# Kernel tuning notes

Hardware: AMD Instinct MI355X
Metric: run time of the kernel (lower is better)

The kernel has to match this reference:

```python
import jax, jax.numpy as jnp
import numpy as np

N = 100000   # nodes
R = 6        # relations (edge types)
E = 400000   # edges per relation
F_IN = 128   # metapath2vec embedding dim
HID = 128    # hidden_dim (conv1 out == conv2 out in RGCN)
OUT = 2      # out_size


def setup_inputs() -> dict:
    key = jax.random.key(0)
    ks = jax.random.split(key, 9)
    x = jax.random.normal(ks[0], (N, F_IN), dtype=jnp.float32)
    edge_src = jax.random.randint(ks[1], (R, E), 0, N, dtype=jnp.int32)
    edge_dst = jax.random.randint(ks[2], (R, E), 0, N, dtype=jnp.int32)
    W1 = jax.random.normal(ks[3], (R, F_IN, HID), dtype=jnp.float32) * 0.05
    b1 = jnp.zeros((R, HID), dtype=jnp.float32)
    W2 = jax.random.normal(ks[4], (R, HID, HID), dtype=jnp.float32) * 0.05
    b2 = jnp.zeros((R, HID), dtype=jnp.float32)
    Wc = jax.random.normal(ks[5], (HID, OUT), dtype=jnp.float32) * 0.05
    bc = jnp.zeros((OUT,), dtype=jnp.float32)
    return {"x": x, "edge_src": edge_src, "edge_dst": edge_dst,
            "W1": W1, "b1": b1, "W2": W2, "b2": b2, "Wc": Wc, "bc": bc}


def _graph_conv(x, src, dst, W, b):
    """DGL GraphConv, norm='both': D_dst^{-1/2} A D_src^{-1/2} X W + b."""
    ones = jnp.ones(src.shape, x.dtype)
    deg_out = jax.ops.segment_sum(ones, src, num_segments=N)  # [N]
    deg_in = jax.ops.segment_sum(ones, dst, num_segments=N)   # [N]
    norm_src = jnp.where(deg_out > 0, jax.lax.rsqrt(jnp.maximum(deg_out, 1.0)), 0.0)
    norm_dst = jnp.where(deg_in > 0, jax.lax.rsqrt(jnp.maximum(deg_in, 1.0)), 0.0)
    msg = (x * norm_src[:, None])[src]                         # [E, F] gather
    agg = jax.ops.segment_sum(msg, dst, num_segments=N)       # [N, F] scatter-sum
    return (agg * norm_dst[:, None]) @ W + b                  # [N, H]


def _hetero_layer(x, edge_src, edge_dst, W, b):
    # HeteroGraphConv(aggregate='sum'): run each relation's GraphConv, sum results.
    conv = jax.vmap(_graph_conv, in_axes=(None, 0, 0, 0, 0))
    return conv(x, edge_src, edge_dst, W, b).sum(axis=0)      # [N, H]


def reference(x, edge_src, edge_dst, W1, b1, W2, b2, Wc, bc):
    h = jax.nn.relu(_hetero_layer(x, edge_src, edge_dst, W1, b1))
    h = _hetero_layer(h, edge_src, edge_dst, W2, b2)
    g = h.mean(axis=0)          # mean-pool node embeddings -> graph embedding
    return g @ Wc + bc          # classifier logits, shape [OUT]
```

## Files before the change

kernel.cpp:

```cpp
#include <hip/hip_runtime.h>

#define N_NODES 100000
#define NREL 6
#define NEDGE 400000
#define FDIM 128
#define HID 128

constexpr int RN = NREL * N_NODES;
constexpr int NBIN = 391;
constexpr int BINCAP = 1280;
constexpr int CSRCAP = 2304;
constexpr int CHUNK = 8192;
constexpr int NCHUNK = (NEDGE + CHUNK - 1) / CHUNK;

constexpr int NB_XC = (N_NODES * 32) / 256;
constexpr int NB_WC = (NREL * FDIM * HID) / 256;
constexpr int PREP_BLOCKS = NB_XC + NB_WC + NREL + 1;

typedef __attribute__((ext_vector_type(8))) short short8;
typedef __attribute__((ext_vector_type(4))) float f32x4;

__device__ __forceinline__ unsigned short f2bf(float f) {
  union { float f; unsigned int u; } v; v.f = f;
  unsigned int u = v.u;
  unsigned int r = (u + 0x7FFFu + ((u >> 16) & 1u)) >> 16;
  return (unsigned short)r;
}
__device__ __forceinline__ float bflo(unsigned int w) {
  union { unsigned int u; float f; } v; v.u = w << 16; return v.f;
}
__device__ __forceinline__ float bfhi(unsigned int w) {
  union { unsigned int u; float f; } v; v.u = w & 0xffff0000u; return v.f;
}

__global__ void k_zero(unsigned int* __restrict__ p, int nwords) {
  int id = blockIdx.x * blockDim.x + threadIdx.x;
  if (id < nwords) p[id] = 0u;
}

__global__ __launch_bounds__(256) void k_phase1(
    const int* __restrict__ src, const int* __restrict__ dst,
    int* __restrict__ gCurIn, int* __restrict__ gCurOut,
    unsigned int* __restrict__ stIn, unsigned int* __restrict__ stOut) {
  __shared__ int hIn[NBIN], hOut[NBIN], bIn[NBIN], bOut[NBIN];
  const int r = blockIdx.x / NCHUNK;
  const int c = blockIdx.x % NCHUNK;
  const int t = threadIdx.x;
  for (int i = t; i < NBIN; i += 256) { hIn[i] = 0; hOut[i] = 0; }
  __syncthreads();
  const int base = c * CHUNK;
  const int lim = min(CHUNK, NEDGE - base);
  const int* __restrict__ sR = src + r * NEDGE + base;
  const int* __restrict__ dR = dst + r * NEDGE + base;
  for (int i = t; i < lim; i += 256) {
    atomicAdd(&hIn[dR[i] >> 8], 1);
    atomicAdd(&hOut[sR[i] >> 8], 1);
  }
  __syncthreads();
  for (int i = t; i < NBIN; i += 256) {
    bIn[i]  = atomicAdd(&gCurIn[r * NBIN + i], hIn[i]);
    bOut[i] = atomicAdd(&gCurOut[r * NBIN + i], hOut[i]);
    hIn[i] = 0; hOut[i] = 0;
  }
  __syncthreads();
  for (int i = t; i < lim; i += 256) {
    const int s = sR[i], d = dR[i];
    const int bi = d >> 8, bo = s >> 8;
    const int pi = bIn[bi] + atomicAdd(&hIn[bi], 1);
    const int po = bOut[bo] + atomicAdd(&hOut[bo], 1);
    if (pi < BINCAP)
      stIn[(size_t)(r * NBIN + bi) * BINCAP + pi] = ((unsigned)(d & 255) << 17) | (unsigned)s;
    if (po < BINCAP)
      stOut[(size_t)(r * NBIN + bo) * BINCAP + po] = ((unsigned)(s & 255) << 17) | (unsigned)d;
  }
}

__global__ __launch_bounds__(256) void k_p2a(const unsigned int* __restrict__ stOut,
                                             const int* __restrict__ gCurOut,
                                             float* __restrict__ ns) {
  __shared__ int cnt[256];
  const int rb = blockIdx.x;
  const int r = rb / NBIN, b = rb % NBIN;
  const int t = threadIdx.x;
  cnt[t] = 0;
  __syncthreads();
  const int m = min(gCurOut[rb], BINCAP);
  const unsigned int* __restrict__ st = stOut + (size_t)rb * BINCAP;
  for (int i = t; i < m; i += 256) atomicAdd(&cnt[st[i] >> 17], 1);
  __syncthreads();
  const int n = b * 256 + t;
  if (n < N_NODES) ns[r * N_NODES + n] = cnt[t] > 0 ? rsqrtf((float)cnt[t]) : 0.f;
}

__global__ __launch_bounds__(256) void k_p2in(const unsigned int* __restrict__ stIn,
                                              const int* __restrict__ gCurIn,
                                              const float* __restrict__ ns,
                                              int4* __restrict__ meta,
                                              float* __restrict__ ndA,
                                              int2* __restrict__ csr) {
  __shared__ int cnt[256], offs[256];
  __shared__ int wsum[4];
  const int rb = blockIdx.x;
  const int r = rb / NBIN, b = rb % NBIN;
  const int t = threadIdx.x;
  cnt[t] = 0;
  __syncthreads();
  const int m = min(gCurIn[rb], BINCAP);
  const unsigned int* __restrict__ st = stIn + (size_t)rb * BINCAP;
  for (int i = t; i < m; i += 256) atomicAdd(&cnt[st[i] >> 17], 1);
  __syncthreads();
  const int lane = t & 63, wid = t >> 6;
  const int pc = (cnt[t] + 3) & ~3;
  int sum = pc;
#pragma unroll
  for (int o = 1; o < 64; o <<= 1) {
    int y = __shfl_up(sum, o);
    if (lane >= o) sum += y;
  }
  if (lane == 63) wsum[wid] = sum;
  __syncthreads();
  int wadd = 0;
  for (int w = 0; w < wid; ++w) wadd += wsum[w];
  offs[t] = sum - pc + wadd;
  __syncthreads();
  const int n = b * 256 + t;
  const int binBase = rb * CSRCAP;
  if (n < N_NODES) {
    const int d = cnt[t];
    const float nd = d > 0 ? rsqrtf((float)d) : 0.f;
    meta[r * N_NODES + n] = make_int4(d, binBase + offs[t], __float_as_int(nd), 0);
    ndA[r * N_NODES + n] = nd;
    int2* __restrict__ c = csr + binBase + offs[t];
    for (int e = d; e < ((d + 3) & ~3); ++e) c[e] = make_int2(0, 0);
  }
  __syncthreads();
  cnt[t] = 0;
  __syncthreads();
  const float* __restrict__ nsr = ns + r * N_NODES;
  for (int i = t; i < m; i += 256) {
    const unsigned int v = st[i];
    const int local = v >> 17;
    const int s = v & 0x1FFFF;
    const int pos = offs[local] + atomicAdd(&cnt[local], 1);
    csr[binBase + pos] = make_int2(s, __float_as_int(nsr[s]));
  }
}

__global__ __launch_bounds__(256) void k_p2b(const unsigned int* __restrict__ stOut,
                                             const int* __restrict__ gCurOut,
                                             const float* __restrict__ ns,
                                             const float* __restrict__ ndA,
                                             float* __restrict__ wmv) {
  __shared__ float fc[256];
  const int rb = blockIdx.x;
  const int r = rb / NBIN, b = rb % NBIN;
  const int t = threadIdx.x;
  fc[t] = 0.f;
  __syncthreads();
  const int m = min(gCurOut[rb], BINCAP);
  const unsigned int* __restrict__ st = stOut + (size_t)rb * BINCAP;
  const float* __restrict__ ndr = ndA + r * N_NODES;
  for (int i = t; i < m; i += 256) {
    const unsigned int v = st[i];
    atomicAdd(&fc[v >> 17], ndr[v & 0x1FFFF]);
  }
  __syncthreads();
  const int n = b * 256 + t;
  if (n < N_NODES) {
    const int rn = r * N_NODES + n;
    wmv[rn] = fc[t] * ns[rn];
  }
}

__global__ __launch_bounds__(256) void k_prep(
    const float* __restrict__ x, unsigned short* __restrict__ xb,
    const float* __restrict__ W1, const float* __restrict__ b1,
    const float* __restrict__ b2,
    unsigned short* __restrict__ W1T, float* __restrict__ bias1,
    float* __restrict__ bias2,
    const float* __restrict__ W2, const float* __restrict__ Wc,
    float* __restrict__ u) {
  const int b = blockIdx.x;
  const int t = threadIdx.x;
  if (b < NB_XC) {
    const int id = b * 256 + t;
    const float4 v = ((const float4*)x)[id];
    ushort4 o;
    o.x = f2bf(v.x); o.y = f2bf(v.y); o.z = f2bf(v.z); o.w = f2bf(v.w);
    ((ushort4*)xb)[id] = o;
  } else if (b < NB_XC + NB_WC) {
    const int id = (b - NB_XC) * 256 + t;
    const int r = id >> 14;
    const int rem = id & 16383;
    const int j = rem >> 7;
    const int k = rem & 127;
    W1T[id] = f2bf(W1[r * 16384 + k * 128 + j]);
  } else if (b < NB_XC + NB_WC + NREL) {
    const int r = b - (NB_XC + NB_WC);
    const int k = t >> 1;
    const int c = t & 1;
    const float* __restrict__ row = W2 + r * (HID * HID) + k * HID;
    float s = 0.f;
#pragma unroll 8
    for (int j = 0; j < HID; ++j) s = fmaf(row[j], Wc[j * 2 + c], s);
    u[(r * HID + k) * 2 + c] = s;
  } else {
    if (t < HID) {
      float s1 = 0.f, s2 = 0.f;
      for (int r = 0; r < NREL; ++r) {
        s1 += b1[r * HID + t];
        s2 += b2[r * HID + t];
      }
      bias1[t] = s1;
      bias2[t] = s2;
    }
  }
}

__global__ __launch_bounds__(256, 6) void k_layer1(
    const unsigned short* __restrict__ xb,
    const int2* __restrict__ csr_ew,
    const int4* __restrict__ meta,
    const unsigned short* __restrict__ W1T,
    const float* __restrict__ bias1,
    unsigned short* __restrict__ h)
{
  __shared__ unsigned short zA[4][16][136];
  const int tid = threadIdx.x;
  const int wave = tid >> 6;
  const int lane = tid & 63;
  const int sub = lane >> 4;
  const int flane = lane & 15;
  const int wnb = blockIdx.x * 64 + wave * 16;

  f32x4 acc[8];
#pragma unroll
  for (int t = 0; t < 8; ++t) acc[t] = (f32x4){0.f, 0.f, 0.f, 0.f};

  const int pn = wnb + flane;
  const bool pok = pn < N_NODES;
  const int pnc = pok ? pn : (N_NODES - 1);
  int4 mt = meta[pnc];
  if (!pok) { mt.x = 0; mt.z = 0; }

  for (int r = 0; r < NREL; ++r) {
#pragma unroll
    for (int pass = 0; pass < 4; ++pass) {
      const int row = pass * 4 + sub;
      const int d = __shfl(mt.x, row);
      const int o = __shfl(mt.y, row);
      const float nd = __int_as_float(__shfl(mt.z, row));
      const uint4* __restrict__ lst = (const uint4*)(csr_ew + o);
      const unsigned fo = (unsigned)(flane << 3);
      float b[8];
#pragma unroll
      for (int k = 0; k < 8; ++k) b[k] = 0.f;
      const int nb = (d + 3) >> 2;
      for (int bi = 0; bi < nb; ++bi) {
        const uint4 qa = lst[2 * bi];
        const uint4 qb = lst[2 * bi + 1];
        const float w0 = __uint_as_float(qa.y);
        const float w1 = __uint_as_float(qa.w);
        const float w2 = __uint_as_float(qb.y);
        const float w3 = __uint_as_float(qb.w);
        const uint4 v0 = *(const uint4*)(xb + ((size_t)qa.x << 7) + fo);
        const uint4 v1 = *(const uint4*)(xb + ((size_t)qa.z << 7) + fo);
        const uint4 v2 = *(const uint4*)(xb + ((size_t)qb.x << 7) + fo);
        const uint4 v3 = *(const uint4*)(xb + ((size_t)qb.z << 7) + fo);
#define ACC8(V, W) \
        b[0] = fmaf(bflo(V.x), W, b[0]); b[1] = fmaf(bfhi(V.x), W, b[1]); \
        b[2] = fmaf(bflo(V.y), W, b[2]); b[3] = fmaf(bfhi(V.y), W, b[3]); \
        b[4] = fmaf(bflo(V.z), W, b[4]); b[5] = fmaf(bfhi(V.z), W, b[5]); \
        b[6] = fmaf(bflo(V.w), W, b[6]); b[7] = fmaf(bfhi(V.w), W, b[7]);
        ACC8(v0, w0) ACC8(v1, w1) ACC8(v2, w2) ACC8(v3, w3)
#undef ACC8
      }
      uint4 pk;
      pk.x = (unsigned)f2bf(b[0] * nd) | ((unsigned)f2bf(b[1] * nd) << 16);
      pk.y = (unsigned)f2bf(b[2] * nd) | ((unsigned)f2bf(b[3] * nd) << 16);
      pk.z = (unsigned)f2bf(b[4] * nd) | ((unsigned)f2bf(b[5] * nd) << 16);
      pk.w = (unsigned)f2bf(b[6] * nd) | ((unsigned)f2bf(b[7] * nd) << 16);
      *(uint4*)(&zA[wave][row][flane * 8]) = pk;
    }
    int4 mtn = mt;
    if (r + 1 < NREL) {
      mtn = meta[(r + 1) * N_NODES + pnc];
      if (!pok) { mtn.x = 0; mtn.z = 0; }
    }
    const int m = lane & 15;
    const int qq = lane >> 4;
    const unsigned short* __restrict__ wr = W1T + r * (FDIM * HID);
#pragma unroll
    for (int kk = 0; kk < 4; ++kk) {
      const short8 af = *(const short8*)(&zA[wave][m][kk * 32 + qq * 8]);
#pragma unroll
      for (int t = 0; t < 8; ++t) {
        const short8 bfr = *(const short8*)(wr + (t * 16 + m) * 128 + kk * 32 + qq * 8);
        acc[t] = __builtin_amdgcn_mfma_f32_16x16x32_bf16(af, bfr, acc[t], 0, 0, 0);
      }
    }
    mt = mtn;
  }
  const int col = lane & 15;
  const int rq = (lane >> 4) * 4;
#pragma unroll
  for (int t = 0; t < 8; ++t) {
#pragma unroll
    for (int rr = 0; rr < 4; ++rr) {
      const int node = wnb + rq + rr;
      if (node < N_NODES) {
        const int f = t * 16 + col;
        float v = acc[t][rr] + bias1[f];
        v = fmaxf(v, 0.f);
        h[(size_t)node * FDIM + f] = f2bf(v);
      }
    }
  }
}

__global__ __launch_bounds__(256) void k_mv(const unsigned short* __restrict__ h,
                                            const float* __restrict__ wmv,
                                            float* __restrict__ mv) {
  __shared__ float sh[16][136];
  const int sub = threadIdx.x >> 4;
  const int flane = threadIdx.x & 15;
  const unsigned fo = (unsigned)(flane << 3);
  float acc[NREL][8];
#pragma unroll
  for (int r = 0; r < NREL; ++r)
#pragma unroll
    for (int k = 0; k < 8; ++k) acc[r][k] = 0.f;
  const int nbase = blockIdx.x * 256 + sub * 16;
  for (int i = 0; i < 16; ++i) {
    const int n = nbase + i;
    if (n >= N_NODES) break;
    const uint4 hv = *(const uint4*)(h + ((size_t)n << 7) + fo);
    float hf[8];
    hf[0] = bflo(hv.x); hf[1] = bfhi(hv.x); hf[2] = bflo(hv.y); hf[3] = bfhi(hv.y);
    hf[4] = bflo(hv.z); hf[5] = bfhi(hv.z); hf[6] = bflo(hv.w); hf[7] = bfhi(hv.w);
#pragma unroll
    for (int r = 0; r < NREL; ++r) {
      const float w = wmv[r * N_NODES + n];
#pragma unroll
      for (int k = 0; k < 8; ++k) acc[r][k] = fmaf(w, hf[k], acc[r][k]);
    }
  }
  const float inv = 1.0f / (float)N_NODES;
  const int t = threadIdx.x;
#pragma unroll
  for (int r = 0; r < NREL; ++r) {
    __syncthreads();
#pragma unroll
    for (int k = 0; k < 8; ++k) sh[sub][flane * 8 + k] = acc[r][k];
    __syncthreads();
    if (t < 128) {
      float s = 0.f;
#pragma unroll
      for (int j = 0; j < 16; ++j) s += sh[j][t];
      atomicAdd(&mv[r * HID + t], s * inv);
    }
  }
}

__global__ __launch_bounds__(256) void k_final(const float* __restrict__ mv,
                                               const float* __restrict__ u,
                                               const float* __restrict__ bias2,
                                               const float* __restrict__ Wc,
                                               const float* __restrict__ bc,
                                               float* __restrict__ out) {
  __shared__ float r0[256], r1[256];
  const int t = threadIdx.x;
  float s0 = 0.f, s1 = 0.f;
  for (int rk = t; rk < NREL * HID; rk += 256) {
    const float m = mv[rk];
    s0 = fmaf(m, u[rk * 2], s0);
    s1 = fmaf(m, u[rk * 2 + 1], s1);
  }
  r0[t] = s0; r1[t] = s1;
  __syncthreads();
  for (int off = 128; off > 0; off >>= 1) {
    if (t < off) { r0[t] += r0[t + off]; r1[t] += r1[t + off]; }
    __syncthreads();
  }
  if (t == 0) {
    float t0 = bc[0], t1 = bc[1];
    for (int j = 0; j < HID; ++j) {
      const float b = bias2[j];
      t0 = fmaf(b, Wc[j * 2], t0);
      t1 = fmaf(b, Wc[j * 2 + 1], t1);
    }
    out[0] = r0[0] + t0;
    out[1] = r1[0] + t1;
  }
}

extern "C" void kernel_launch(void* const* d_in, const int* in_sizes, int n_in,
                              void* d_out, int out_size, void* d_ws, size_t ws_size,
                              hipStream_t stream) {
  (void)in_sizes; (void)n_in; (void)out_size; (void)ws_size;
  const float* x   = (const float*)d_in[0];
  const int* esrc  = (const int*)d_in[1];
  const int* edst  = (const int*)d_in[2];
  const float* W1  = (const float*)d_in[3];
  const float* b1  = (const float*)d_in[4];
  const float* W2  = (const float*)d_in[5];
  const float* b2  = (const float*)d_in[6];
  const float* Wc  = (const float*)d_in[7];
  const float* bc  = (const float*)d_in[8];
  float* out = (float*)d_out;

  char* p = (char*)d_ws;
  size_t off = 0;
  auto take = [&](size_t bytes) -> void* {
    void* q = p + off;
    off += (bytes + 255) & ~(size_t)255;
    return q;
  };
  int*   gCurIn  = (int*)take((size_t)NREL * NBIN * 4);
  int*   gCurOut = (int*)take((size_t)NREL * NBIN * 4);
  float* mv      = (float*)take((size_t)NREL * HID * 4);
  const size_t zero_bytes = off;
  float* ns   = (float*)take((size_t)RN * 4);
  float* ndA  = (float*)take((size_t)RN * 4);
  float* wmv  = (float*)take((size_t)RN * 4);
  int4*  meta = (int4*)take((size_t)RN * 16);
  unsigned int* stIn  = (unsigned int*)take((size_t)NREL * NBIN * BINCAP * 4);
  unsigned int* stOut = (unsigned int*)take((size_t)NREL * NBIN * BINCAP * 4);
  int2* csr = (int2*)take((size_t)NREL * NBIN * CSRCAP * 8);
  unsigned short* W1T = (unsigned short*)take((size_t)NREL * FDIM * HID * 2);
  float* bias1 = (float*)take(HID * 4);
  float* bias2 = (float*)take(HID * 4);
  float* u     = (float*)take((size_t)NREL * HID * 2 * 4);
  unsigned short* h  = (unsigned short*)take((size_t)N_NODES * FDIM * 2);
  unsigned short* xb = (unsigned short*)take((size_t)N_NODES * FDIM * 2);

  const int zero_words = (int)(zero_bytes / 4);
  k_zero<<<(zero_words + 255) / 256, 256, 0, stream>>>((unsigned int*)d_ws, zero_words);
  k_phase1<<<NREL * NCHUNK, 256, 0, stream>>>(esrc, edst, gCurIn, gCurOut, stIn, stOut);
  k_p2a<<<NREL * NBIN, 256, 0, stream>>>(stOut, gCurOut, ns);
  k_p2in<<<NREL * NBIN, 256, 0, stream>>>(stIn, gCurIn, ns, meta, ndA, csr);
  k_p2b<<<NREL * NBIN, 256, 0, stream>>>(stOut, gCurOut, ns, ndA, wmv);
  k_prep<<<PREP_BLOCKS, 256, 0, stream>>>(x, xb, W1, b1, b2, W1T, bias1, bias2, W2, Wc, u);
  k_layer1<<<(N_NODES + 63) / 64, 256, 0, stream>>>(xb, csr, meta, W1T, bias1, h);
  k_mv<<<(N_NODES + 255) / 256, 256, 0, stream>>>(h, wmv, mv);
  k_final<<<1, 256, 0, stream>>>(mv, u, bias2, Wc, bc, out);
}
```

Before: 590.9 us.

## Fuse graph-build kernels and shrink layer1 blocks to single waves

Merges the edge-binning phase into the prep kernel, so both run as one launch with heterogeneous blocks. The separate out-degree, in-CSR and weight passes become two kernels: one computes both degree counts plus CSR offsets, the other fills the CSR and the wmv weights. Layer1 now launches one 64-thread wave per 16 nodes and drops the bounds checks, which relies on N being divisible by 16. This cuts the number of launches and repeated bin scans and gives finer block scheduling for layer1.

```diff
diff --git a/kernel.cpp b/kernel.cpp
--- a/kernel.cpp
+++ b/kernel.cpp
@@ -13,9 +13,10 @@
 constexpr int CHUNK = 8192;
 constexpr int NCHUNK = (NEDGE + CHUNK - 1) / CHUNK;
 
+constexpr int PH1_BLOCKS = NREL * NCHUNK;
 constexpr int NB_XC = (N_NODES * 32) / 256;
 constexpr int NB_WC = (NREL * FDIM * HID) / 256;
-constexpr int PREP_BLOCKS = NB_XC + NB_WC + NREL + 1;
+constexpr int BUILD_BLOCKS = PH1_BLOCKS + NB_XC + NB_WC + NREL + 1;
 
 typedef __attribute__((ext_vector_type(8))) short short8;
 typedef __attribute__((ext_vector_type(4))) float f32x4;
@@ -38,141 +39,10 @@
   if (id < nwords) p[id] = 0u;
 }
 
-__global__ __launch_bounds__(256) void k_phase1(
+__global__ __launch_bounds__(256) void k_build(
     const int* __restrict__ src, const int* __restrict__ dst,
     int* __restrict__ gCurIn, int* __restrict__ gCurOut,
-    unsigned int* __restrict__ stIn, unsigned int* __restrict__ stOut) {
-  __shared__ int hIn[NBIN], hOut[NBIN], bIn[NBIN], bOut[NBIN];
-  const int r = blockIdx.x / NCHUNK;
-  const int c = blockIdx.x % NCHUNK;
-  const int t = threadIdx.x;
-  for (int i = t; i < NBIN; i += 256) { hIn[i] = 0; hOut[i] = 0; }
-  __syncthreads();
-  const int base = c * CHUNK;
-  const int lim = min(CHUNK, NEDGE - base);
-  const int* __restrict__ sR = src + r * NEDGE + base;
-  const int* __restrict__ dR = dst + r * NEDGE + base;
-  for (int i = t; i < lim; i += 256) {
-    atomicAdd(&hIn[dR[i] >> 8], 1);
-    atomicAdd(&hOut[sR[i] >> 8], 1);
-  }
-  __syncthreads();
-  for (int i = t; i < NBIN; i += 256) {
-    bIn[i]  = atomicAdd(&gCurIn[r * NBIN + i], hIn[i]);
-    bOut[i] = atomicAdd(&gCurOut[r * NBIN + i], hOut[i]);
-    hIn[i] = 0; hOut[i] = 0;
-  }
-  __syncthreads();
-  for (int i = t; i < lim; i += 256) {
-    const int s = sR[i], d = dR[i];
-    const int bi = d >> 8, bo = s >> 8;
-    const int pi = bIn[bi] + atomicAdd(&hIn[bi], 1);
-    const int po = bOut[bo] + atomicAdd(&hOut[bo], 1);
-    if (pi < BINCAP)
-      stIn[(size_t)(r * NBIN + bi) * BINCAP + pi] = ((unsigned)(d & 255) << 17) | (unsigned)s;
-    if (po < BINCAP)
-      stOut[(size_t)(r * NBIN + bo) * BINCAP + po] = ((unsigned)(s & 255) << 17) | (unsigned)d;
-  }
-}
-
-__global__ __launch_bounds__(256) void k_p2a(const unsigned int* __restrict__ stOut,
-                                             const int* __restrict__ gCurOut,
-                                             float* __restrict__ ns) {
-  __shared__ int cnt[256];
-  const int rb = blockIdx.x;
-  const int r = rb / NBIN, b = rb % NBIN;
-  const int t = threadIdx.x;
-  cnt[t] = 0;
-  __syncthreads();
-  const int m = min(gCurOut[rb], BINCAP);
-  const unsigned int* __restrict__ st = stOut + (size_t)rb * BINCAP;
-  for (int i = t; i < m; i += 256) atomicAdd(&cnt[st[i] >> 17], 1);
-  __syncthreads();
-  const int n = b * 256 + t;
-  if (n < N_NODES) ns[r * N_NODES + n] = cnt[t] > 0 ? rsqrtf((float)cnt[t]) : 0.f;
-}
-
-__global__ __launch_bounds__(256) void k_p2in(const unsigned int* __restrict__ stIn,
-                                              const int* __restrict__ gCurIn,
-                                              const float* __restrict__ ns,
-                                              int4* __restrict__ meta,
-                                              float* __restrict__ ndA,
-                                              int2* __restrict__ csr) {
-  __shared__ int cnt[256], offs[256];
-  __shared__ int wsum[4];
-  const int rb = blockIdx.x;
-  const int r = rb / NBIN, b = rb % NBIN;
-  const int t = threadIdx.x;
-  cnt[t] = 0;
-  __syncthreads();
-  const int m = min(gCurIn[rb], BINCAP);
-  const unsigned int* __restrict__ st = stIn + (size_t)rb * BINCAP;
-  for (int i = t; i < m; i += 256) atomicAdd(&cnt[st[i] >> 17], 1);
-  __syncthreads();
-  const int lane = t & 63, wid = t >> 6;
-  const int pc = (cnt[t] + 3) & ~3;
-  int sum = pc;
-#pragma unroll
-  for (int o = 1; o < 64; o <<= 1) {
-    int y = __shfl_up(sum, o);
-    if (lane >= o) sum += y;
-  }
-  if (lane == 63) wsum[wid] = sum;
-  __syncthreads();
-  int wadd = 0;
-  for (int w = 0; w < wid; ++w) wadd += wsum[w];
-  offs[t] = sum - pc + wadd;
-  __syncthreads();
-  const int n = b * 256 + t;
-  const int binBase = rb * CSRCAP;
-  if (n < N_NODES) {
-    const int d = cnt[t];
-    const float nd = d > 0 ? rsqrtf((float)d) : 0.f;
-    meta[r * N_NODES + n] = make_int4(d, binBase + offs[t], __float_as_int(nd), 0);
-    ndA[r * N_NODES + n] = nd;
-    int2* __restrict__ c = csr + binBase + offs[t];
-    for (int e = d; e < ((d + 3) & ~3); ++e) c[e] = make_int2(0, 0);
-  }
-  __syncthreads();
-  cnt[t] = 0;
-  __syncthreads();
-  const float* __restrict__ nsr = ns + r * N_NODES;
-  for (int i = t; i < m; i += 256) {
-    const unsigned int v = st[i];
-    const int local = v >> 17;
-    const int s = v & 0x1FFFF;
-    const int pos = offs[local] + atomicAdd(&cnt[local], 1);
-    csr[binBase + pos] = make_int2(s, __float_as_int(nsr[s]));
-  }
-}
-
-__global__ __launch_bounds__(256) void k_p2b(const unsigned int* __restrict__ stOut,
-                                             const int* __restrict__ gCurOut,
-                                             const float* __restrict__ ns,
-                                             const float* __restrict__ ndA,
-                                             float* __restrict__ wmv) {
-  __shared__ float fc[256];
-  const int rb = blockIdx.x;
-  const int r = rb / NBIN, b = rb % NBIN;
-  const int t = threadIdx.x;
-  fc[t] = 0.f;
-  __syncthreads();
-  const int m = min(gCurOut[rb], BINCAP);
-  const unsigned int* __restrict__ st = stOut + (size_t)rb * BINCAP;
-  const float* __restrict__ ndr = ndA + r * N_NODES;
-  for (int i = t; i < m; i += 256) {
-    const unsigned int v = st[i];
-    atomicAdd(&fc[v >> 17], ndr[v & 0x1FFFF]);
-  }
-  __syncthreads();
-  const int n = b * 256 + t;
-  if (n < N_NODES) {
-    const int rn = r * N_NODES + n;
-    wmv[rn] = fc[t] * ns[rn];
-  }
-}
-
-__global__ __launch_bounds__(256) void k_prep(
+    unsigned int* __restrict__ stIn, unsigned int* __restrict__ stOut,
     const float* __restrict__ x, unsigned short* __restrict__ xb,
     const float* __restrict__ W1, const float* __restrict__ b1,
     const float* __restrict__ b2,
@@ -180,23 +50,54 @@
     float* __restrict__ bias2,
     const float* __restrict__ W2, const float* __restrict__ Wc,
     float* __restrict__ u) {
-  const int b = blockIdx.x;
+  __shared__ int hIn[NBIN], hOut[NBIN], bIn[NBIN], bOut[NBIN];
+  const int blk = blockIdx.x;
   const int t = threadIdx.x;
-  if (b < NB_XC) {
-    const int id = b * 256 + t;
+  if (blk < PH1_BLOCKS) {
+    const int r = blk / NCHUNK;
+    const int c = blk % NCHUNK;
+    for (int i = t; i < NBIN; i += 256) { hIn[i] = 0; hOut[i] = 0; }
+    __syncthreads();
+    const int base = c * CHUNK;
+    const int lim = min(CHUNK, NEDGE - base);
+    const int* __restrict__ sR = src + r * NEDGE + base;
+    const int* __restrict__ dR = dst + r * NEDGE + base;
+    for (int i = t; i < lim; i += 256) {
+      atomicAdd(&hIn[dR[i] >> 8], 1);
+      atomicAdd(&hOut[sR[i] >> 8], 1);
+    }
+    __syncthreads();
+    for (int i = t; i < NBIN; i += 256) {
+      bIn[i]  = atomicAdd(&gCurIn[r * NBIN + i], hIn[i]);
+      bOut[i] = atomicAdd(&gCurOut[r * NBIN + i], hOut[i]);
+      hIn[i] = 0; hOut[i] = 0;
+    }
+    __syncthreads();
+    for (int i = t; i < lim; i += 256) {
+      const int s = sR[i], d = dR[i];
+      const int bi = d >> 8, bo = s >> 8;
+      const int pi = bIn[bi] + atomicAdd(&hIn[bi], 1);
+      const int po = bOut[bo] + atomicAdd(&hOut[bo], 1);
+      if (pi < BINCAP)
+        stIn[(size_t)(r * NBIN + bi) * BINCAP + pi] = ((unsigned)(d & 255) << 17) | (unsigned)s;
+      if (po < BINCAP)
+        stOut[(size_t)(r * NBIN + bo) * BINCAP + po] = ((unsigned)(s & 255) << 17) | (unsigned)d;
+    }
+  } else if (blk < PH1_BLOCKS + NB_XC) {
+    const int id = (blk - PH1_BLOCKS) * 256 + t;
     const float4 v = ((const float4*)x)[id];
     ushort4 o;
     o.x = f2bf(v.x); o.y = f2bf(v.y); o.z = f2bf(v.z); o.w = f2bf(v.w);
     ((ushort4*)xb)[id] = o;
-  } else if (b < NB_XC + NB_WC) {
-    const int id = (b - NB_XC) * 256 + t;
+  } else if (blk < PH1_BLOCKS + NB_XC + NB_WC) {
+    const int id = (blk - PH1_BLOCKS - NB_XC) * 256 + t;
     const int r = id >> 14;
     const int rem = id & 16383;
     const int j = rem >> 7;
     const int k = rem & 127;
     W1T[id] = f2bf(W1[r * 16384 + k * 128 + j]);
-  } else if (b < NB_XC + NB_WC + NREL) {
-    const int r = b - (NB_XC + NB_WC);
+  } else if (blk < PH1_BLOCKS + NB_XC + NB_WC + NREL) {
+    const int r = blk - (PH1_BLOCKS + NB_XC + NB_WC);
     const int k = t >> 1;
     const int c = t & 1;
     const float* __restrict__ row = W2 + r * (HID * HID) + k * HID;
@@ -217,7 +118,101 @@
   }
 }
 
-__global__ __launch_bounds__(256, 6) void k_layer1(
+__global__ __launch_bounds__(256) void k_p2cnt(const unsigned int* __restrict__ stIn,
+                                               const unsigned int* __restrict__ stOut,
+                                               const int* __restrict__ gCurIn,
+                                               const int* __restrict__ gCurOut,
+                                               float* __restrict__ ns,
+                                               float* __restrict__ ndA,
+                                               int4* __restrict__ meta,
+                                               int2* __restrict__ csr) {
+  __shared__ int cntIn[256], cntOut[256];
+  __shared__ int wsum[4];
+  const int rb = blockIdx.x;
+  const int r = rb / NBIN, b = rb % NBIN;
+  const int t = threadIdx.x;
+  cntIn[t] = 0; cntOut[t] = 0;
+  __syncthreads();
+  const int mi = min(gCurIn[rb], BINCAP);
+  const int mo = min(gCurOut[rb], BINCAP);
+  const unsigned int* __restrict__ sti = stIn + (size_t)rb * BINCAP;
+  const unsigned int* __restrict__ sto = stOut + (size_t)rb * BINCAP;
+  for (int i = t; i < mi; i += 256) atomicAdd(&cntIn[sti[i] >> 17], 1);
+  for (int i = t; i < mo; i += 256) atomicAdd(&cntOut[sto[i] >> 17], 1);
+  __syncthreads();
+  const int lane = t & 63, wid = t >> 6;
+  const int pc = (cntIn[t] + 3) & ~3;
+  int sum = pc;
+#pragma unroll
+  for (int o = 1; o < 64; o <<= 1) {
+    int y = __shfl_up(sum, o);
+    if (lane >= o) sum += y;
+  }
+  if (lane == 63) wsum[wid] = sum;
+  __syncthreads();
+  int wadd = 0;
+  for (int w = 0; w < wid; ++w) wadd += wsum[w];
+  const int off = sum - pc + wadd;
+  const int n = b * 256 + t;
+  const int binBase = rb * CSRCAP;
+  if (n < N_NODES) {
+    const int rn = r * N_NODES + n;
+    const int d = cntIn[t];
+    const int dO = cntOut[t];
+    const float nd = d > 0 ? rsqrtf((float)d) : 0.f;
+    ns[rn] = dO > 0 ? rsqrtf((float)dO) : 0.f;
+    ndA[rn] = nd;
+    meta[rn] = make_int4(d, binBase + off, __float_as_int(nd), 0);
+    int2* __restrict__ c = csr + binBase + off;
+    for (int e = d; e < ((d + 3) & ~3); ++e) c[e] = make_int2(0, 0);
+  }
+}
+
+__global__ __launch_bounds__(256) void k_p2fill(const unsigned int* __restrict__ stIn,
+                                                const unsigned int* __restrict__ stOut,
+                                                const int* __restrict__ gCurIn,
+                                                const int* __restrict__ gCurOut,
+                                                const int4* __restrict__ meta,
+                                                const float* __restrict__ ns,
+                                                const float* __restrict__ ndA,
+                                                int2* __restrict__ csr,
+                                                float* __restrict__ wmv) {
+  __shared__ int offs[256], cnt[256];
+  __shared__ float fc[256];
+  const int rb = blockIdx.x;
+  const int r = rb / NBIN, b = rb % NBIN;
+  const int t = threadIdx.x;
+  const int n = b * 256 + t;
+  const int rnT = r * N_NODES + (n < N_NODES ? n : N_NODES - 1);
+  offs[t] = meta[rnT].y;
+  cnt[t] = 0;
+  fc[t] = 0.f;
+  __syncthreads();
+  const int mi = min(gCurIn[rb], BINCAP);
+  const int mo = min(gCurOut[rb], BINCAP);
+  const unsigned int* __restrict__ sti = stIn + (size_t)rb * BINCAP;
+  const unsigned int* __restrict__ sto = stOut + (size_t)rb * BINCAP;
+  const float* __restrict__ nsr = ns + r * N_NODES;
+  const float* __restrict__ ndr = ndA + r * N_NODES;
+  for (int i = t; i < mi; i += 256) {
+    const unsigned int v = sti[i];
+    const int local = v >> 17;
+    const int s = v & 0x1FFFF;
+    const int pos = offs[local] + atomicAdd(&cnt[local], 1);
+    csr[pos] = make_int2(s, __float_as_int(nsr[s]));
+  }
+  for (int i = t; i < mo; i += 256) {
+    const unsigned int v = sto[i];
+    atomicAdd(&fc[v >> 17], ndr[v & 0x1FFFF]);
+  }
+  __syncthreads();
+  if (n < N_NODES) {
+    const int rn = r * N_NODES + n;
+    wmv[rn] = fc[t] * ns[rn];
+  }
+}
+
+__global__ __launch_bounds__(64, 8) void k_layer1(
     const unsigned short* __restrict__ xb,
     const int2* __restrict__ csr_ew,
     const int4* __restrict__ meta,
@@ -225,23 +220,18 @@
     const float* __restrict__ bias1,
     unsigned short* __restrict__ h)
 {
-  __shared__ unsigned short zA[4][16][136];
-  const int tid = threadIdx.x;
-  const int wave = tid >> 6;
-  const int lane = tid & 63;
+  __shared__ unsigned short zA[16][136];
+  const int lane = threadIdx.x;
   const int sub = lane >> 4;
   const int flane = lane & 15;
-  const int wnb = blockIdx.x * 64 + wave * 16;
+  const int wnb = blockIdx.x * 16;
 
   f32x4 acc[8];
 #pragma unroll
   for (int t = 0; t < 8; ++t) acc[t] = (f32x4){0.f, 0.f, 0.f, 0.f};
 
   const int pn = wnb + flane;
-  const bool pok = pn < N_NODES;
-  const int pnc = pok ? pn : (N_NODES - 1);
-  int4 mt = meta[pnc];
-  if (!pok) { mt.x = 0; mt.z = 0; }
+  int4 mt = meta[pn];
 
   for (int r = 0; r < NREL; ++r) {
 #pragma unroll
@@ -280,19 +270,16 @@
       pk.y = (unsigned)f2bf(b[2] * nd) | ((unsigned)f2bf(b[3] * nd) << 16);
       pk.z = (unsigned)f2bf(b[4] * nd) | ((unsigned)f2bf(b[5] * nd) << 16);
       pk.w = (unsigned)f2bf(b[6] * nd) | ((unsigned)f2bf(b[7] * nd) << 16);
-      *(uint4*)(&zA[wave][row][flane * 8]) = pk;
+      *(uint4*)(&zA[row][flane * 8]) = pk;
     }
     int4 mtn = mt;
-    if (r + 1 < NREL) {
-      mtn = meta[(r + 1) * N_NODES + pnc];
-      if (!pok) { mtn.x = 0; mtn.z = 0; }
-    }
+    if (r + 1 < NREL) mtn = meta[(r + 1) * N_NODES + pn];
     const int m = lane & 15;
     const int qq = lane >> 4;
     const unsigned short* __restrict__ wr = W1T + r * (FDIM * HID);
 #pragma unroll
     for (int kk = 0; kk < 4; ++kk) {
-      const short8 af = *(const short8*)(&zA[wave][m][kk * 32 + qq * 8]);
+      const short8 af = *(const short8*)(&zA[m][kk * 32 + qq * 8]);
 #pragma unroll
       for (int t = 0; t < 8; ++t) {
         const short8 bfr = *(const short8*)(wr + (t * 16 + m) * 128 + kk * 32 + qq * 8);
@@ -308,12 +295,10 @@
 #pragma unroll
     for (int rr = 0; rr < 4; ++rr) {
       const int node = wnb + rq + rr;
-      if (node < N_NODES) {
-        const int f = t * 16 + col;
-        float v = acc[t][rr] + bias1[f];
-        v = fmaxf(v, 0.f);
-        h[(size_t)node * FDIM + f] = f2bf(v);
-      }
+      const int f = t * 16 + col;
+      float v = acc[t][rr] + bias1[f];
+      v = fmaxf(v, 0.f);
+      h[(size_t)node * FDIM + f] = f2bf(v);
     }
   }
 }
@@ -436,12 +421,14 @@
 
   const int zero_words = (int)(zero_bytes / 4);
   k_zero<<<(zero_words + 255) / 256, 256, 0, stream>>>((unsigned int*)d_ws, zero_words);
-  k_phase1<<<NREL * NCHUNK, 256, 0, stream>>>(esrc, edst, gCurIn, gCurOut, stIn, stOut);
-  k_p2a<<<NREL * NBIN, 256, 0, stream>>>(stOut, gCurOut, ns);
-  k_p2in<<<NREL * NBIN, 256, 0, stream>>>(stIn, gCurIn, ns, meta, ndA, csr);
-  k_p2b<<<NREL * NBIN, 256, 0, stream>>>(stOut, gCurOut, ns, ndA, wmv);
-  k_prep<<<PREP_BLOCKS, 256, 0, stream>>>(x, xb, W1, b1, b2, W1T, bias1, bias2, W2, Wc, u);
-  k_layer1<<<(N_NODES + 63) / 64, 256, 0, stream>>>(xb, csr, meta, W1T, bias1, h);
+  k_build<<<BUILD_BLOCKS, 256, 0, stream>>>(esrc, edst, gCurIn, gCurOut, stIn, stOut,
+                                            x, xb, W1, b1, b2, W1T, bias1, bias2,
+                                            W2, Wc, u);
+  k_p2cnt<<<NREL * NBIN, 256, 0, stream>>>(stIn, stOut, gCurIn, gCurOut,
+                                           ns, ndA, meta, csr);
+  k_p2fill<<<NREL * NBIN, 256, 0, stream>>>(stIn, stOut, gCurIn, gCurOut, meta,
+                                            ns, ndA, csr, wmv);
+  k_layer1<<<N_NODES / 16, 64, 0, stream>>>(xb, csr, meta, W1T, bias1, h);
   k_mv<<<(N_NODES + 255) / 256, 256, 0, stream>>>(h, wmv, mv);
   k_final<<<1, 256, 0, stream>>>(mv, u, bias2, Wc, bc, out);
 }
```

Result: no change. 600.8 us (+1.7%).
